# Optimization experiments

Hardware: AMD Instinct MI355X
Metric: run time of the kernel (lower is better)

Reference implementation:

```python
import jax, jax.numpy as jnp
import numpy as np

DIM = 1024
HEADS = 16
HEAD_DIM = DIM // HEADS
EPS = 1e-6

def _layernorm(x, gamma, beta):
    # LayerNorm over last axis (head_dim), biased variance like torch
    mu = jnp.mean(x, axis=-1, keepdims=True)
    var = jnp.mean(jnp.square(x - mu), axis=-1, keepdims=True)
    return (x - mu) * jax.lax.rsqrt(var + EPS) * gamma + beta

def setup_inputs() -> dict:
    key = jax.random.key(0)
    ks = jax.random.split(key, 12)
    B, N, D = 2, 2048, DIM
    s = 1.0 / np.sqrt(D)
    inp = {
        'x': jax.random.normal(ks[0], (B, N, D), jnp.float32),
        'attn_bias': jax.random.normal(ks[1], (B, 1, N, N), jnp.float32),
        'Wq': jax.random.normal(ks[2], (D, D), jnp.float32) * s,
        'bq': jnp.zeros((D,), jnp.float32),
        'Wk': jax.random.normal(ks[3], (D, D), jnp.float32) * s,
        'bk': jnp.zeros((D,), jnp.float32),
        'Wv': jax.random.normal(ks[4], (D, D), jnp.float32) * s,
        'bv': jnp.zeros((D,), jnp.float32),
        'Wo': jax.random.normal(ks[5], (D, D), jnp.float32) * s,
        'bo': jnp.zeros((D,), jnp.float32),
        'q_gamma': jnp.ones((HEAD_DIM,), jnp.float32),
        'q_beta': jnp.zeros((HEAD_DIM,), jnp.float32),
        'k_gamma': jnp.ones((HEAD_DIM,), jnp.float32),
        'k_beta': jnp.zeros((HEAD_DIM,), jnp.float32),
    }
    return inp

def reference(x, attn_bias, Wq, bq, Wk, bk, Wv, bv, Wo, bo, q_gamma, q_beta, k_gamma, k_beta):
    B, N, D = x.shape
    h, dh = HEADS, HEAD_DIM
    # QKV projections (torch Linear: x @ W.T + b) -> (B, h, N, dh)
    def proj(W, b):
        y = jnp.einsum('bnd,ed->bne', x, W) + b
        return y.reshape(B, N, h, dh).transpose(0, 2, 1, 3)
    q = proj(Wq, bq)
    k = proj(Wk, bk)
    v = proj(Wv, bv)
    # per-head LayerNorm on Q and K
    q = _layernorm(q, q_gamma, q_beta)
    k = _layernorm(k, k_gamma, k_beta)
    # scaled dot-product attention with additive graph bias
    scores = jnp.einsum('bhnd,bhmd->bhnm', q, k) / np.sqrt(dh).astype(np.float32)
    scores = scores + attn_bias  # (B,1,N,N) broadcasts over heads
    attn = jax.nn.softmax(scores, axis=-1)
    out = jnp.einsum('bhnm,bhmd->bhnd', attn, v)
    out = out.transpose(0, 2, 1, 3).reshape(B, N, D)
    return jnp.einsum('bnd,ed->bne', out, Wo) + bo
```

## Files before the change

### kernel.cpp

```cpp
#include <hip/hip_runtime.h>
#include <hip/hip_bf16.h>
#include <hip/hip_fp16.h>

#define D_MODEL 1024
#define N_SEQ   2048
#define N_B     2
#define M_ROWS  (N_B * N_SEQ)

typedef __attribute__((ext_vector_type(8))) short bf16x8;
typedef __attribute__((ext_vector_type(4))) float f32x4;

typedef const __attribute__((address_space(1))) unsigned int gu32_t;
typedef __attribute__((address_space(3))) unsigned int lu32_t;

__device__ __forceinline__ void gload16(const void* g, void* l) {
  __builtin_amdgcn_global_load_lds((gu32_t*)g, (lu32_t*)l, 16, 0, 0);
}

__device__ inline unsigned short f2bf(float f) {
  union { float f; unsigned int u; } v; v.f = f;
  unsigned int r = (v.u + 0x7FFFu + ((v.u >> 16) & 1u)) >> 16;
  return (unsigned short)r;
}

__device__ __forceinline__ unsigned int cvt_pk_bf16(float a, float b) {
  unsigned int r;
  asm("v_cvt_pk_bf16_f32 %0, %1, %2" : "=v"(r) : "v"(a), "v"(b));
  return r;
}

__device__ __forceinline__ float exp2fast(float x) {
#if __has_builtin(__builtin_amdgcn_exp2f)
  return __builtin_amdgcn_exp2f(x);
#else
  return __expf(x * 0.69314718056f);
#endif
}

#define WAITV(N) asm volatile("s_waitcnt vmcnt(" #N ")" ::: "memory")

__device__ __forceinline__ int lds_off(int row, int col ) {
  return row * 64 + (((col >> 3) ^ (row & 7)) << 3) + (col & 7);
}

template<int ROWS, int NTHR = 256>
__device__ __forceinline__ void stage_tile(const unsigned short* gbase, size_t gstride,
                                           unsigned short* lds, int tid) {
  const int wave = tid >> 6;
#pragma unroll
  for (int rnd = 0; rnd < ROWS * 8 / NTHR; ++rnd) {
    int c = rnd * NTHR + tid;
    int row = c >> 3, pc = c & 7;
    int gcol = ((pc ^ (row & 7)) << 3);
    gload16(gbase + (size_t)row * gstride + gcol,
            lds + (size_t)(rnd * NTHR + wave * 64) * 8);
  }
}

__device__ __forceinline__ void stage_bias(const unsigned short* gbase,
                                           unsigned short* lds, int tid) {
  const int wave = tid >> 6;
#pragma unroll
  for (int rnd = 0; rnd < 2; ++rnd) {
    int c = rnd * 512 + tid;
    int row = c >> 3, pc = c & 7;
    gload16(gbase + (size_t)row * N_SEQ + pc * 8,
            lds + (size_t)(rnd * 512 + wave * 64) * 8);
  }
}

constexpr size_t XEL = (size_t)M_ROWS * D_MODEL;
constexpr size_t WEL = (size_t)D_MODEL * D_MODEL;
constexpr size_t BEL = (size_t)N_B * N_SEQ * N_SEQ;
constexpr size_t TOTEL = XEL + 4 * WEL + BEL;

__launch_bounds__(256)
__global__ void cvt_kernel(const float* __restrict__ x, const float* __restrict__ bias,
                           const float* __restrict__ wq, const float* __restrict__ wk,
                           const float* __restrict__ wv, const float* __restrict__ wo,
                           unsigned short* __restrict__ dst,
                           unsigned short* __restrict__ dstB) {
  size_t i = ((size_t)blockIdx.x * 256 + threadIdx.x) * 8;
  if (i >= TOTEL) return;
  if (i >= XEL + 4 * WEL) {
    size_t off = i - (XEL + 4 * WEL);
    int row = (int)(off >> 11);
    int key = (int)(off & 2047);
    constexpr float LOG2E = 1.44269504088896340736f;
    float4 f0 = *(const float4*)(bias + off);
    float4 f1 = *(const float4*)(bias + off + 4);
    __half t[8] = { __float2half(f0.x * LOG2E), __float2half(f0.y * LOG2E),
                    __float2half(f0.z * LOG2E), __float2half(f0.w * LOG2E),
                    __float2half(f1.x * LOG2E), __float2half(f1.y * LOG2E),
                    __float2half(f1.z * LOG2E), __float2half(f1.w * LOG2E) };
    int j  = (key >> 3) & 7;
    int jp = j ^ ((row >> 1) & 7);
    uint4 v = *(const uint4*)t;
    if (row & 1) { uint4 w; w.x = v.z; w.y = v.w; w.z = v.x; w.w = v.y; v = w; }
    *(uint4*)(dstB + (((size_t)row << 11) + (key & ~63) + jp * 8)) = v;
    return;
  }
  const float* s; size_t off = i;
  if (off < XEL)                { s = x; }
  else if (off < XEL + WEL)     { s = wq; off -= XEL; }
  else if (off < XEL + 2*WEL)   { s = wk; off -= XEL + WEL; }
  else if (off < XEL + 3*WEL)   { s = wv; off -= XEL + 2*WEL; }
  else                          { s = wo; off -= XEL + 3*WEL; }
  float4 f0 = *(const float4*)(s + off);
  float4 f1 = *(const float4*)(s + off + 4);
  unsigned short t[8] = { f2bf(f0.x), f2bf(f0.y), f2bf(f0.z), f2bf(f0.w),
                          f2bf(f1.x), f2bf(f1.y), f2bf(f1.z), f2bf(f1.w) };
  *(uint4*)(dst + i) = *(const uint4*)t;
}

__device__ __forceinline__ void mainloop128(const unsigned short* __restrict__ A,
                                            const unsigned short* __restrict__ Bw,
                                            int m0, int e0,
                                            unsigned short* As, unsigned short* Bs,
                                            f32x4 (&acc)[4][4]) {
  const int tid  = threadIdx.x;
  const int wave = tid >> 6, lane = tid & 63;
  const int l16 = lane & 15, quad = lane >> 4;
  const int wr = wave >> 1, wc = wave & 1;

  for (int kt = 0; kt < D_MODEL / 64; ++kt) {
    const int k0 = kt * 64;
    stage_tile<128>(A + (size_t)m0 * D_MODEL + k0, D_MODEL, As, tid);
    stage_tile<128>(Bw + (size_t)e0 * D_MODEL + k0, D_MODEL, Bs, tid);
    __syncthreads();
#pragma unroll
    for (int ks = 0; ks < 2; ++ks) {
      bf16x8 af[4], bfr[4];
#pragma unroll
      for (int mi = 0; mi < 4; ++mi)
        af[mi] = *(const bf16x8*)(As + lds_off(wr * 64 + mi * 16 + l16, ks * 32 + quad * 8));
#pragma unroll
      for (int ci = 0; ci < 4; ++ci)
        bfr[ci] = *(const bf16x8*)(Bs + lds_off(wc * 64 + ci * 16 + l16, ks * 32 + quad * 8));
#pragma unroll
      for (int mi = 0; mi < 4; ++mi)
#pragma unroll
        for (int ci = 0; ci < 4; ++ci)
          acc[mi][ci] = __builtin_amdgcn_mfma_f32_16x16x32_bf16(af[mi], bfr[ci], acc[mi][ci], 0, 0, 0);
    }
    __syncthreads();
  }
}

__launch_bounds__(256)
__global__ void qkv_gemm(const unsigned short* __restrict__ xb,
                         const unsigned short* __restrict__ wb,
                         const float* __restrict__ bq, const float* __restrict__ bk,
                         const float* __restrict__ bv,
                         const float* __restrict__ qg, const float* __restrict__ qbeta,
                         const float* __restrict__ kg, const float* __restrict__ kbeta,
                         unsigned short* __restrict__ qkout,
                         unsigned short* __restrict__ vt) {
  __shared__ unsigned short As[128 * 64];
  __shared__ unsigned short Bs[128 * 64];
  const int m0  = blockIdx.x * 128;
  const int by  = blockIdx.y;
  const int mat = by >> 3;
  const int e0  = (by & 7) * 128;
  const unsigned short* Bw = wb + (size_t)mat * WEL;

  f32x4 acc[4][4];
#pragma unroll
  for (int mi = 0; mi < 4; ++mi)
#pragma unroll
    for (int ci = 0; ci < 4; ++ci) acc[mi][ci] = f32x4{0.f, 0.f, 0.f, 0.f};

  mainloop128(xb, Bw, m0, e0, As, Bs, acc);

  const int lane = threadIdx.x & 63, wave = threadIdx.x >> 6;
  const int l16 = lane & 15, quad = lane >> 4;
  const int wr = wave >> 1, wc = wave & 1;
  const int colbase = e0 + wc * 64;

  const float* bias = (mat == 0) ? bq : ((mat == 1) ? bk : bv);
  float bcol[4];
#pragma unroll
  for (int ci = 0; ci < 4; ++ci) bcol[ci] = bias[colbase + ci * 16 + l16];
#pragma unroll
  for (int mi = 0; mi < 4; ++mi)
#pragma unroll
    for (int ci = 0; ci < 4; ++ci)
#pragma unroll
      for (int r = 0; r < 4; ++r) acc[mi][ci][r] += bcol[ci];

  if (mat < 2) {
    const float* gamma = (mat == 0) ? qg : kg;
    const float* beta  = (mat == 0) ? qbeta : kbeta;
    const float sc = (mat == 0) ? 0.18033688011112042f : 1.0f;
    float g4[4], bt4[4];
#pragma unroll
    for (int ci = 0; ci < 4; ++ci) {
      g4[ci] = gamma[ci * 16 + l16] * sc;
      bt4[ci] = beta[ci * 16 + l16] * sc;
    }
#pragma unroll
    for (int mi = 0; mi < 4; ++mi)
#pragma unroll
      for (int r = 0; r < 4; ++r) {
        float s = acc[mi][0][r] + acc[mi][1][r] + acc[mi][2][r] + acc[mi][3][r];
        s += __shfl_xor(s, 1); s += __shfl_xor(s, 2);
        s += __shfl_xor(s, 4); s += __shfl_xor(s, 8);
        float mean = s * (1.f / 64.f);
        float d0 = acc[mi][0][r] - mean, d1 = acc[mi][1][r] - mean;
        float d2 = acc[mi][2][r] - mean, d3 = acc[mi][3][r] - mean;
        float q = d0 * d0 + d1 * d1 + d2 * d2 + d3 * d3;
        q += __shfl_xor(q, 1); q += __shfl_xor(q, 2);
        q += __shfl_xor(q, 4); q += __shfl_xor(q, 8);
        float rs = rsqrtf(q * (1.f / 64.f) + 1e-6f);
        acc[mi][0][r] = d0 * rs * g4[0] + bt4[0];
        acc[mi][1][r] = d1 * rs * g4[1] + bt4[1];
        acc[mi][2][r] = d2 * rs * g4[2] + bt4[2];
        acc[mi][3][r] = d3 * rs * g4[3] + bt4[3];
      }
    unsigned short* out = qkout + (size_t)mat * XEL;
#pragma unroll
    for (int mi = 0; mi < 4; ++mi)
#pragma unroll
      for (int ci = 0; ci < 4; ++ci) {
        int col = colbase + ci * 16 + l16;
#pragma unroll
        for (int r = 0; r < 4; ++r) {
          int row = m0 + wr * 64 + mi * 16 + quad * 4 + r;
          out[(size_t)row * D_MODEL + col] = f2bf(acc[mi][ci][r]);
        }
      }
  } else {
    unsigned short* scr = ((wave < 2) ? As : Bs) + (size_t)(wave & 1) * 4096;
#pragma unroll
    for (int ci = 0; ci < 4; ++ci) {
      int dl = ci * 16 + l16;
      int sw = (dl & 3) * 16;
#pragma unroll
      for (int mi = 0; mi < 4; ++mi)
#pragma unroll
        for (int r = 0; r < 4; ++r) {
          int np = ((mi >> 1) << 5) + (quad << 3) + ((mi & 1) << 2) + r;
          scr[dl * 64 + (np ^ sw)] = f2bf(acc[mi][ci][r]);
        }
    }
    __builtin_amdgcn_wave_barrier();
    int row0 = m0 + wr * 64;
    int b = row0 >> 11, nb = row0 & 2047;
    int h = colbase >> 6;
    int dl = lane;
    unsigned short* gdst = vt + ((size_t)((b * 16 + h) * 64 + dl) * N_SEQ + nb);
    const unsigned short* srow = scr + dl * 64;
    int sw = (dl & 3) * 16;
#pragma unroll
    for (int j = 0; j < 8; ++j) {
      uint4 vv = *(const uint4*)(srow + ((j * 8) ^ sw));
      *(uint4*)(gdst + j * 8) = vv;
    }
  }
}

__launch_bounds__(256)
__global__ void out_gemm(const unsigned short* __restrict__ ao,
                         const unsigned short* __restrict__ wob,
                         const float* __restrict__ bo,
                         float* __restrict__ out) {
  __shared__ unsigned short As[128 * 64];
  __shared__ unsigned short Bs[128 * 64];
  const int m0 = blockIdx.x * 128;
  const int e0 = blockIdx.y * 128;

  f32x4 acc[4][4];
#pragma unroll
  for (int mi = 0; mi < 4; ++mi)
#pragma unroll
    for (int ci = 0; ci < 4; ++ci) acc[mi][ci] = f32x4{0.f, 0.f, 0.f, 0.f};

  mainloop128(ao, wob, m0, e0, As, Bs, acc);

  const int lane = threadIdx.x & 63, wave = threadIdx.x >> 6;
  const int l16 = lane & 15, quad = lane >> 4;
  const int wr = wave >> 1, wc = wave & 1;
  float bcol[4];
#pragma unroll
  for (int ci = 0; ci < 4; ++ci) bcol[ci] = bo[e0 + wc * 64 + ci * 16 + l16];
#pragma unroll
  for (int mi = 0; mi < 4; ++mi)
#pragma unroll
    for (int ci = 0; ci < 4; ++ci) {
      int col = e0 + wc * 64 + ci * 16 + l16;
#pragma unroll
      for (int r = 0; r < 4; ++r) {
        int row = m0 + wr * 64 + mi * 16 + quad * 4 + r;
        out[(size_t)row * D_MODEL + col] = acc[mi][ci][r] + bcol[ci];
      }
    }
}

__launch_bounds__(512, 4)
__global__ void attn_kernel(const unsigned short* __restrict__ Q,
                            const unsigned short* __restrict__ Kn,
                            const unsigned short* __restrict__ Vt,
                            const unsigned short* __restrict__ bias16,
                            unsigned short* __restrict__ Out) {
  __shared__ unsigned short smem[36864];

  const int tid  = threadIdx.x;
  const int wave = tid >> 6, lane = tid & 63;
  const int quad = lane >> 4, l16 = lane & 15;
  const int pairId = wave >> 1;
  const int kh = wave & 1;
  const int bidx0 = blockIdx.x;
  const int bidx = (bidx0 & 7) * 64 + (bidx0 >> 3);
  const int qt = bidx & 15;
  const int h  = (bidx >> 4) & 15;
  const int b  = bidx >> 8;
  const int q0 = qt * 128;
  const size_t base  = (size_t)b * N_SEQ * D_MODEL + (size_t)h * 64;
  const unsigned short* vtb = Vt + (size_t)(b * 16 + h) * 64 * N_SEQ;
  const unsigned short* bbase = bias16 + ((size_t)b * N_SEQ + q0) * N_SEQ;

  stage_tile<128, 512>(Q + base + (size_t)q0 * D_MODEL, D_MODEL, smem, tid);
  __syncthreads();

  bf16x8 aq[2][2];
#pragma unroll
  for (int mi = 0; mi < 2; ++mi)
#pragma unroll
    for (int ks = 0; ks < 2; ++ks)
      aq[mi][ks] = *(const bf16x8*)(smem + lds_off(pairId * 32 + mi * 16 + l16, ks * 32 + quad * 8));
  __syncthreads();

  stage_tile<64, 512>(Kn + base, D_MODEL, smem, tid);
  stage_tile<64, 512>(vtb, N_SEQ, smem + 12288, tid);
  stage_bias(bbase, smem + 20480, tid);
  stage_tile<64, 512>(Kn + base + (size_t)64 * D_MODEL, D_MODEL,
                      smem + 4096, tid);

  WAITV(1);
  __builtin_amdgcn_s_barrier();
  __builtin_amdgcn_sched_barrier(0);

  f32x4 o[2][4];
#pragma unroll
  for (int mi = 0; mi < 2; ++mi)
#pragma unroll
    for (int cd = 0; cd < 4; ++cd) o[mi][cd] = f32x4{0.f, 0.f, 0.f, 0.f};
  float lsum[2] = {0.f, 0.f};

  constexpr int NT = N_SEQ / 64;
  for (int kt = 0; kt < NT; ++kt) {
    unsigned short* Kcur = smem + (kt % 3) * 4096;
    unsigned short* Vcur = smem + 12288 + (kt & 1) * 4096;
    const unsigned short* Bcur = smem + 20480 + (kt & 1) * 8192;

    if (kt + 2 < NT)
      stage_tile<64, 512>(Kn + base + (size_t)(kt + 2) * 64 * D_MODEL, D_MODEL,
                          smem + ((kt + 2) % 3) * 4096, tid);
    if (kt + 1 < NT) {
      stage_tile<64, 512>(vtb + (kt + 1) * 64, N_SEQ,
                          smem + 12288 + ((kt + 1) & 1) * 4096, tid);
      stage_bias(bbase + (kt + 1) * 64, smem + 20480 + ((kt + 1) & 1) * 8192, tid);
    }
    if (kt < NT - 2)      { WAITV(4); }
    else if (kt == NT - 2){ WAITV(3); }
    else                  { WAITV(0); }

    f32x4 zb[2][2];
#pragma unroll
    for (int mi = 0; mi < 2; ++mi)
#pragma unroll
      for (int cl = 0; cl < 2; ++cl) {
        uint2 bw = *(const uint2*)(Bcur + (pairId * 32 + mi * 16 + l16) * 64 +
                                   (((kh * 8 + quad + cl * 4) ^ l16) << 2));
        float2 fa = __half22float2(*(const __half2*)&bw.x);
        float2 fb = __half22float2(*(const __half2*)&bw.y);
        zb[mi][cl] = f32x4{fa.x, fa.y, fb.x, fb.y};
      }

    f32x4 sfT[2][2];
#pragma unroll
    for (int cl = 0; cl < 2; ++cl) {
      const int c = kh * 2 + cl;
      bf16x8 k0 = *(const bf16x8*)(Kcur + lds_off(c * 16 + l16, quad * 8));
      bf16x8 k1 = *(const bf16x8*)(Kcur + lds_off(c * 16 + l16, 32 + quad * 8));
      __builtin_amdgcn_s_setprio(1);
#pragma unroll
      for (int mi = 0; mi < 2; ++mi) {
        f32x4 z = __builtin_amdgcn_mfma_f32_16x16x32_bf16(k0, aq[mi][0], zb[mi][cl], 0, 0, 0);
        sfT[mi][cl] = __builtin_amdgcn_mfma_f32_16x16x32_bf16(k1, aq[mi][1], z, 0, 0, 0);
      }
      __builtin_amdgcn_s_setprio(0);
    }

    union PafU { unsigned int w[4]; bf16x8 v; };
    PafU paf[2];
#pragma unroll
    for (int mi = 0; mi < 2; ++mi)
#pragma unroll
      for (int cl = 0; cl < 2; ++cl) {
        float p0 = exp2fast(sfT[mi][cl][0]);
        float p1 = exp2fast(sfT[mi][cl][1]);
        float p2 = exp2fast(sfT[mi][cl][2]);
        float p3 = exp2fast(sfT[mi][cl][3]);
        lsum[mi] += (p0 + p1) + (p2 + p3);
        paf[mi].w[cl * 2]     = cvt_pk_bf16(p0, p1);
        paf[mi].w[cl * 2 + 1] = cvt_pk_bf16(p2, p3);
      }

    {
      bf16x8 bv[4];
#pragma unroll
      for (int cd = 0; cd < 4; ++cd)
        bv[cd] = *(const bf16x8*)(Vcur + lds_off(cd * 16 + l16, kh * 32 + quad * 8));
      __builtin_amdgcn_s_setprio(1);
#pragma unroll
      for (int mi = 0; mi < 2; ++mi)
#pragma unroll
        for (int cd = 0; cd < 4; ++cd)
          o[mi][cd] = __builtin_amdgcn_mfma_f32_16x16x32_bf16(bv[cd], paf[mi].v, o[mi][cd], 0, 0, 0);
      __builtin_amdgcn_s_setprio(0);
    }

    if (kt + 1 < NT) {
      __builtin_amdgcn_s_barrier();
      __builtin_amdgcn_sched_barrier(0);
    }
  }

  WAITV(0);
  __syncthreads();

  float* red = (float*)smem;
  float* slot = red + (size_t)(pairId * 64 + lane) * 34;
  if (kh) {
#pragma unroll
    for (int mi = 0; mi < 2; ++mi)
#pragma unroll
      for (int cd = 0; cd < 4; ++cd)
#pragma unroll
        for (int r = 0; r < 4; ++r)
          slot[mi * 16 + cd * 4 + r] = o[mi][cd][r];
    slot[32] = lsum[0];
    slot[33] = lsum[1];
  }
  __syncthreads();
  if (!kh) {
#pragma unroll
    for (int mi = 0; mi < 2; ++mi)
#pragma unroll
      for (int cd = 0; cd < 4; ++cd)
#pragma unroll
        for (int r = 0; r < 4; ++r)
          o[mi][cd][r] += slot[mi * 16 + cd * 4 + r];
    lsum[0] += slot[32];
    lsum[1] += slot[33];

#pragma unroll
    for (int mi = 0; mi < 2; ++mi) {
      float l = lsum[mi];
      l += __shfl_xor(l, 16);
      l += __shfl_xor(l, 32);
      float inv = 1.0f / l;
      size_t row = (size_t)b * N_SEQ + q0 + pairId * 32 + mi * 16 + l16;
#pragma unroll
      for (int cd = 0; cd < 4; ++cd) {
        uint2 vv;
        vv.x = cvt_pk_bf16(o[mi][cd][0] * inv, o[mi][cd][1] * inv);
        vv.y = cvt_pk_bf16(o[mi][cd][2] * inv, o[mi][cd][3] * inv);
        *(uint2*)(Out + row * D_MODEL + h * 64 + cd * 16 + quad * 4) = vv;
      }
    }
  }
}

extern "C" void kernel_launch(void* const* d_in, const int* in_sizes, int n_in,
                              void* d_out, int out_size, void* d_ws, size_t ws_size,
                              hipStream_t stream) {
  const float* x    = (const float*)d_in[0];
  const float* bias = (const float*)d_in[1];
  const float* Wq = (const float*)d_in[2];  const float* bq = (const float*)d_in[3];
  const float* Wk = (const float*)d_in[4];  const float* bk = (const float*)d_in[5];
  const float* Wv = (const float*)d_in[6];  const float* bv = (const float*)d_in[7];
  const float* Wo = (const float*)d_in[8];  const float* bo = (const float*)d_in[9];
  const float* qg = (const float*)d_in[10]; const float* qb = (const float*)d_in[11];
  const float* kg = (const float*)d_in[12]; const float* kb = (const float*)d_in[13];
  float* out = (float*)d_out;

  unsigned short* wsb = (unsigned short*)d_ws;
  unsigned short* xb  = wsb;
  unsigned short* wqb = wsb + XEL;
  unsigned short* wob = wsb + XEL + 3 * WEL;
  unsigned short* qn  = wsb + XEL + 4 * WEL;
  unsigned short* kn  = qn + XEL;
  unsigned short* vt  = qn + 2 * XEL;
  unsigned short* b16 = qn + 3 * XEL;
  unsigned short* ao  = xb;

  dim3 blk(256, 1, 1);

  cvt_kernel<<<dim3((unsigned)(TOTEL / (256 * 8)), 1, 1), blk, 0, stream>>>(
      x, bias, Wq, Wk, Wv, Wo, wsb, b16);

  qkv_gemm<<<dim3(M_ROWS / 128, 24, 1), blk, 0, stream>>>(
      xb, wqb, bq, bk, bv, qg, qb, kg, kb, qn, vt);

  attn_kernel<<<dim3(N_B * 16 * (N_SEQ / 128), 1, 1), dim3(512, 1, 1), 0, stream>>>(
      qn, kn, vt, b16, ao);

  out_gemm<<<dim3(M_ROWS / 128, D_MODEL / 128, 1), blk, 0, stream>>>(ao, wob, bo, out);
}
```

Measured before the change: 232.9 us.

## Double-buffer LDS tiles in QKV and output GEMM mainloop

The shared GEMM mainloop now uses two LDS buffers per operand and prefetches the next K-tile with async global-to-LDS loads while computing on the current one. This replaces the two block-wide syncs per iteration with one barrier, aiming to hide global load latency. It also raises wave priority around the MFMA block. LDS use per block doubles to 64KB, which may reduce occupancy.

Result: faster. 224.1 us (-3.8%).

```diff
diff --git a/kernel.cpp b/kernel.cpp
--- a/kernel.cpp
+++ b/kernel.cpp
@@ -116,18 +116,36 @@
 __device__ __forceinline__ void mainloop128(const unsigned short* __restrict__ A,
                                             const unsigned short* __restrict__ Bw,
                                             int m0, int e0,
-                                            unsigned short* As, unsigned short* Bs,
+                                            unsigned short* smem,
                                             f32x4 (&acc)[4][4]) {
   const int tid  = threadIdx.x;
   const int wave = tid >> 6, lane = tid & 63;
   const int l16 = lane & 15, quad = lane >> 4;
   const int wr = wave >> 1, wc = wave & 1;
-
-  for (int kt = 0; kt < D_MODEL / 64; ++kt) {
-    const int k0 = kt * 64;
-    stage_tile<128>(A + (size_t)m0 * D_MODEL + k0, D_MODEL, As, tid);
-    stage_tile<128>(Bw + (size_t)e0 * D_MODEL + k0, D_MODEL, Bs, tid);
-    __syncthreads();
+  constexpr int NT = D_MODEL / 64;
+
+  stage_tile<128>(A + (size_t)m0 * D_MODEL, D_MODEL, smem, tid);
+  stage_tile<128>(Bw + (size_t)e0 * D_MODEL, D_MODEL, smem + 16384, tid);
+  WAITV(0);
+  __builtin_amdgcn_s_barrier();
+  __builtin_amdgcn_sched_barrier(0);
+
+  for (int kt = 0; kt < NT; ++kt) {
+    const int cur = kt & 1;
+    unsigned short* As = smem + cur * 8192;
+    unsigned short* Bs = smem + 16384 + cur * 8192;
+
+    if (kt + 1 < NT) {
+      const int nb = cur ^ 1;
+      stage_tile<128>(A + (size_t)m0 * D_MODEL + (kt + 1) * 64, D_MODEL,
+                      smem + nb * 8192, tid);
+      stage_tile<128>(Bw + (size_t)e0 * D_MODEL + (kt + 1) * 64, D_MODEL,
+                      smem + 16384 + nb * 8192, tid);
+      WAITV(8);
+    } else {
+      WAITV(0);
+    }
+
 #pragma unroll
     for (int ks = 0; ks < 2; ++ks) {
       bf16x8 af[4], bfr[4];
@@ -137,14 +155,21 @@
 #pragma unroll
       for (int ci = 0; ci < 4; ++ci)
         bfr[ci] = *(const bf16x8*)(Bs + lds_off(wc * 64 + ci * 16 + l16, ks * 32 + quad * 8));
+      __builtin_amdgcn_s_setprio(1);
 #pragma unroll
       for (int mi = 0; mi < 4; ++mi)
 #pragma unroll
         for (int ci = 0; ci < 4; ++ci)
           acc[mi][ci] = __builtin_amdgcn_mfma_f32_16x16x32_bf16(af[mi], bfr[ci], acc[mi][ci], 0, 0, 0);
-    }
-    __syncthreads();
-  }
+      __builtin_amdgcn_s_setprio(0);
+    }
+
+    if (kt + 1 < NT) {
+      __builtin_amdgcn_s_barrier();
+      __builtin_amdgcn_sched_barrier(0);
+    }
+  }
+  __syncthreads();
 }
 
 __launch_bounds__(256)
@@ -156,8 +181,7 @@
                          const float* __restrict__ kg, const float* __restrict__ kbeta,
                          unsigned short* __restrict__ qkout,
                          unsigned short* __restrict__ vt) {
-  __shared__ unsigned short As[128 * 64];
-  __shared__ unsigned short Bs[128 * 64];
+  __shared__ unsigned short smem[32768];
   const int m0  = blockIdx.x * 128;
   const int by  = blockIdx.y;
   const int mat = by >> 3;
@@ -170,7 +194,7 @@
 #pragma unroll
     for (int ci = 0; ci < 4; ++ci) acc[mi][ci] = f32x4{0.f, 0.f, 0.f, 0.f};
 
-  mainloop128(xb, Bw, m0, e0, As, Bs, acc);
+  mainloop128(xb, Bw, m0, e0, smem, acc);
 
   const int lane = threadIdx.x & 63, wave = threadIdx.x >> 6;
   const int l16 = lane & 15, quad = lane >> 4;
@@ -230,7 +254,7 @@
         }
       }
   } else {
-    unsigned short* scr = ((wave < 2) ? As : Bs) + (size_t)(wave & 1) * 4096;
+    unsigned short* scr = smem + (size_t)wave * 4096;
 #pragma unroll
     for (int ci = 0; ci < 4; ++ci) {
       int dl = ci * 16 + l16;
@@ -264,8 +288,7 @@
                          const unsigned short* __restrict__ wob,
                          const float* __restrict__ bo,
                          float* __restrict__ out) {
-  __shared__ unsigned short As[128 * 64];
-  __shared__ unsigned short Bs[128 * 64];
+  __shared__ unsigned short smem[32768];
   const int m0 = blockIdx.x * 128;
   const int e0 = blockIdx.y * 128;
 
@@ -275,7 +298,7 @@
 #pragma unroll
     for (int ci = 0; ci < 4; ++ci) acc[mi][ci] = f32x4{0.f, 0.f, 0.f, 0.f};
 
-  mainloop128(ao, wob, m0, e0, As, Bs, acc);
+  mainloop128(ao, wob, m0, e0, smem, acc);
 
   const int lane = threadIdx.x & 63, wave = threadIdx.x >> 6;
   const int l16 = lane & 15, quad = lane >> 4;
```
